# Kernel tuning notes

Hardware: AMD Instinct MI355X
Metric: run time of the kernel (lower is better)

## Reference

```python
import jax, jax.numpy as jnp
import numpy as np

N_HEADS = 16

def _rotate_half(t):
    d = t.shape[-1] // 2
    return jnp.concatenate([-t[..., d:], t[..., :d]], axis=-1)

def _apply_rope(t, cos, sin):
    # t: [B,S,H,dh], cos/sin: [S,1,dh] broadcast over B and H
    return t * cos + _rotate_half(t) * sin

def setup_inputs() -> dict:
    key = jax.random.key(0)
    ks = jax.random.split(key, 7)
    B, S, D = 2, 2048, 2048
    dh = D // N_HEADS
    scale = 1.0 / np.sqrt(D)
    return {
        "x": jax.random.normal(ks[0], (B, S, D), dtype=jnp.float32),
        "rope_cos": jax.random.uniform(ks[1], (S, dh), dtype=jnp.float32),
        "rope_sin": jax.random.uniform(ks[2], (S, dh), dtype=jnp.float32),
        "Wq": jax.random.normal(ks[3], (D, D), dtype=jnp.float32) * scale,
        "Wk": jax.random.normal(ks[4], (D, D), dtype=jnp.float32) * scale,
        "Wv": jax.random.normal(ks[5], (D, D), dtype=jnp.float32) * scale,
        "Wo": jax.random.normal(ks[6], (D, D), dtype=jnp.float32) * scale,
    }

def reference(x, rope_cos, rope_sin, Wq, Wk, Wv, Wo):
    B, S, D = x.shape
    H = N_HEADS
    dh = D // H
    # QKV projections (nn.Linear: x @ W.T), reshape to heads
    q = (x @ Wq.T).reshape(B, S, H, dh)
    k = (x @ Wk.T).reshape(B, S, H, dh)
    v = (x @ Wv.T).reshape(B, S, H, dh)
    cos = rope_cos[:, None, :]  # [S,1,dh]
    sin = rope_sin[:, None, :]
    q = _apply_rope(q, cos, sin)
    k = _apply_rope(k, cos, sin)
    # Attention: [B,H,S,S] scores, scaled softmax
    scores = jnp.einsum("bqhd,bkhd->bhqk", q, k) / jnp.sqrt(jnp.asarray(dh, dtype=x.dtype))
    probs = jax.nn.softmax(scores, axis=-1)
    out = jnp.einsum("bhqk,bkhd->bqhd", probs, v).reshape(B, S, D)
    return out @ Wo.T
```

## Files before the change

### kernel.cpp

```cpp
#include <hip/hip_runtime.h>
#include <hip/hip_bf16.h>

typedef unsigned short u16;
typedef __bf16 bf16x8 __attribute__((ext_vector_type(8)));
typedef float f32x4 __attribute__((ext_vector_type(4)));

__device__ __forceinline__ float bf2f(u16 u) {
  union { unsigned int i; float f; } v; v.i = ((unsigned int)u) << 16; return v.f;
}
__device__ __forceinline__ u16 f2bf(float f) {
  union { float f; unsigned int i; } v; v.f = f;
  unsigned int r = v.i + 0x7fffu + ((v.i >> 16) & 1u);
  return (u16)(r >> 16);
}
__device__ __forceinline__ unsigned cvtpk(float lo, float hi) {
  unsigned r;
  asm("v_cvt_pk_bf16_f32 %0, %1, %2" : "=v"(r) : "v"(lo), "v"(hi));
  return r;
}

__device__ __forceinline__ void async_load16(void* lds, const void* g) {
  __builtin_amdgcn_global_load_lds((const __attribute__((address_space(1))) void*)g,
                                   (__attribute__((address_space(3))) void*)lds, 16, 0, 0);
}

__global__ void convert_all(const float* __restrict__ x, const float* __restrict__ Wq,
                            const float* __restrict__ Wk, const float* __restrict__ Wv,
                            const float* __restrict__ Wo, u16* __restrict__ xb,
                            u16* __restrict__ Wqkb, u16* __restrict__ Wvb,
                            u16* __restrict__ Wob) {
  int bid = blockIdx.x;
  const float* src;
  u16* dst;
  int off;
  if (bid < 8192)       { src = x;  dst = xb;              off = bid; }
  else if (bid < 12288) { src = Wq; dst = Wqkb;            off = bid - 8192; }
  else if (bid < 16384) { src = Wk; dst = Wqkb + 4194304;  off = bid - 12288; }
  else if (bid < 20480) { src = Wv; dst = Wvb;             off = bid - 16384; }
  else                  { src = Wo; dst = Wob;             off = bid - 20480; }
  int i = off * 1024 + threadIdx.x * 4;
  float4 v = *(const float4*)(src + i);
  ushort4 o;
  o.x = f2bf(v.x); o.y = f2bf(v.y); o.z = f2bf(v.z); o.w = f2bf(v.w);
  *(ushort4*)(dst + i) = o;
}

template <int OUT_F32, int ROPE>
__device__ __forceinline__ void gemm_tile_body(const u16* __restrict__ A,
                                               const u16* __restrict__ Bm,
                                               void* __restrict__ C, int M, int N, int K,
                                               int swz, u16* sA, u16* sB,
                                               const float* __restrict__ cosb,
                                               const float* __restrict__ sinb,
                                               float qscale) {
  const int nTn = N >> 7;
  int tm = swz / nTn, tn = swz % nTn;
  const int t = threadIdx.x;
  const int w = t >> 6, l = t & 63;
  const int wr = w >> 1, wc = w & 1;
  const int lr = l & 15, lh = l >> 4;
  const size_t row0 = (size_t)tm * 128, col0 = (size_t)tn * 128;

  f32x4 zero = {0.f, 0.f, 0.f, 0.f};
  f32x4 acc[4][4];
#pragma unroll
  for (int i = 0; i < 4; ++i)
#pragma unroll
    for (int j = 0; j < 4; ++j) acc[i][j] = zero;

  const u16* Ag = A + row0 * K;
  const u16* Bg = Bm + col0 * K;

  for (int k0 = 0; k0 < K; k0 += 32) {
#pragma unroll
    for (int i = 0; i < 2; ++i) {
      int c = i * 256 + t;
      int r = c >> 2, kk = (c & 3) << 3;
      async_load16(sA + (((size_t)i * 256 + w * 64) << 3), Ag + (size_t)r * K + k0 + kk);
      async_load16(sB + (((size_t)i * 256 + w * 64) << 3), Bg + (size_t)r * K + k0 + kk);
    }
    __syncthreads();
    bf16x8 af[4], bfr[4];
#pragma unroll
    for (int mi = 0; mi < 4; ++mi)
      af[mi] = *reinterpret_cast<const bf16x8*>(sA + (wr * 64 + mi * 16 + lr) * 32 + lh * 8);
#pragma unroll
    for (int ni = 0; ni < 4; ++ni) {
      int colf = wc * 32 + (ni & 1) * 16 + (ni >> 1) * 64;
      bfr[ni] = *reinterpret_cast<const bf16x8*>(sB + (colf + lr) * 32 + lh * 8);
    }
#pragma unroll
    for (int mi = 0; mi < 4; ++mi)
#pragma unroll
      for (int ni = 0; ni < 4; ++ni)
        acc[mi][ni] = __builtin_amdgcn_mfma_f32_16x16x32_bf16(af[mi], bfr[ni], acc[mi][ni], 0, 0, 0);
    __syncthreads();
  }

  if (ROPE) {
    float scale = (tn < 16) ? qscale : 1.0f;
#pragma unroll
    for (int mi = 0; mi < 4; ++mi)
#pragma unroll
      for (int r = 0; r < 4; ++r) {
        size_t row = row0 + wr * 64 + mi * 16 + lh * 4 + r;
        int s = (int)(row & 2047);
        const float* cr = cosb + s * 128;
        const float* sr = sinb + s * 128;
#pragma unroll
        for (int ni = 0; ni < 2; ++ni) {
          int dlo = wc * 32 + ni * 16 + lr;
          float v0 = acc[mi][ni][r];
          float v1 = acc[mi][ni + 2][r];
          float o0 = (v0 * cr[dlo] - v1 * sr[dlo]) * scale;
          float o1 = (v1 * cr[64 + dlo] + v0 * sr[64 + dlo]) * scale;
          ((u16*)C)[row * N + col0 + dlo]      = f2bf(o0);
          ((u16*)C)[row * N + col0 + 64 + dlo] = f2bf(o1);
        }
      }
  } else {
#pragma unroll
    for (int mi = 0; mi < 4; ++mi)
#pragma unroll
      for (int ni = 0; ni < 4; ++ni)
#pragma unroll
        for (int r = 0; r < 4; ++r) {
          size_t row = row0 + wr * 64 + mi * 16 + lh * 4 + r;
          size_t col = col0 + wc * 32 + (ni & 1) * 16 + (ni >> 1) * 64 + lr;
          float v = acc[mi][ni][r];
          if (OUT_F32)
            ((float*)C)[row * N + col] = v;
          else
            ((u16*)C)[row * N + col] = f2bf(v);
        }
  }
}

__global__ __launch_bounds__(256)
void gemm_qkv(const u16* __restrict__ xb, const u16* __restrict__ Wqkb,
              const u16* __restrict__ Wvb, u16* __restrict__ QKb, u16* __restrict__ VTb,
              const float* __restrict__ cosb, const float* __restrict__ sinb, float qscale) {
  __shared__ __align__(16) u16 sA[128 * 32];
  __shared__ __align__(16) u16 sB[128 * 32];
  int bid = blockIdx.x;
  if (bid < 1024) {
    int swz = (bid & 7) * 128 + (bid >> 3);
    gemm_tile_body<0, 1>(xb, Wqkb, QKb, 4096, 4096, 2048, swz, sA, sB, cosb, sinb, qscale);
  } else {
    int b2 = bid - 1024;
    int swz = (b2 & 7) * 64 + (b2 >> 3);
    gemm_tile_body<0, 0>(Wvb, xb, VTb, 2048, 4096, 2048, swz, sA, sB, nullptr, nullptr, 0.f);
  }
}

__global__ __launch_bounds__(256)
void gemm_o(const u16* __restrict__ Ob, const u16* __restrict__ Wob, float* __restrict__ out) {
  __shared__ __align__(16) u16 sA[128 * 32];
  __shared__ __align__(16) u16 sB[128 * 32];
  int bid = blockIdx.x;
  int swz = (bid & 7) * 64 + (bid >> 3);
  gemm_tile_body<1, 0>(Ob, Wob, (void*)out, 4096, 2048, 2048, swz, sA, sB, nullptr, nullptr, 0.f);
}

__global__ __launch_bounds__(256, 2)
void attn_kernel(const u16* __restrict__ QKb, const u16* __restrict__ VT,
                 u16* __restrict__ Ob) {
  __shared__ __align__(16) u16 sK[2][64 * 128];
  __shared__ __align__(16) u16 sV[2][128 * 64];
  __shared__ __align__(16) u16 sP[4][32 * 64];

  int id = blockIdx.x;
  int swz = (id & 7) * 64 + (id >> 3);
  int bh = swz >> 4;
  int qb = swz & 15;
  int b = bh >> 4, h = bh & 15;
  int t = threadIdx.x, w = t >> 6, l = t & 63;
  int lr = l & 15, lh = l >> 4;
  int lr7 = lr & 7;
  int q0 = qb * 128;

  const u16* Kbase = QKb + (size_t)(b * 2048) * 4096 + 2048 + h * 128;
  const u16* Vbase = VT + (size_t)(h * 128) * 4096 + b * 2048;
  u16* sPw = sP[w];

  bf16x8 aq[2][4];
#pragma unroll
  for (int qf = 0; qf < 2; ++qf) {
    size_t qrow = (size_t)(b * 2048 + q0 + w * 32 + qf * 16 + lr) * 4096 + h * 128;
#pragma unroll
    for (int c = 0; c < 4; ++c)
      aq[qf][c] = *reinterpret_cast<const bf16x8*>(QKb + qrow + c * 32 + lh * 8);
  }

  f32x4 zero = {0.f, 0.f, 0.f, 0.f};
  f32x4 acc_o[2][8];
#pragma unroll
  for (int qf = 0; qf < 2; ++qf)
#pragma unroll
    for (int d = 0; d < 8; ++d) acc_o[qf][d] = zero;
  float m_row[2] = {-1e30f, -1e30f};
  float l_row[2] = {0.f, 0.f};

  auto stage = [&](int buf, int kt2) {
    const u16* Kt = Kbase + (size_t)(kt2 * 64) * 4096;
    const u16* Vt = Vbase + kt2 * 64;
#pragma unroll
    for (int it = 0; it < 4; ++it) {
      int o = it * 4096 + t * 16;
      int rowK = o >> 8;
      int cbK = (o & 255) ^ ((rowK & 7) << 4);
      async_load16((u16*)sK[buf] + (o >> 1), Kt + (size_t)rowK * 4096 + (cbK >> 1));
      int rowV = o >> 7;
      int cbV = (o & 127) ^ ((rowV & 7) << 4);
      async_load16((u16*)sV[buf] + (o >> 1), Vt + (size_t)rowV * 4096 + (cbV >> 1));
    }
  };

  stage(0, 0);
  __syncthreads();
  int cur = 0;

  for (int kt = 0; kt < 32; ++kt) {
    if (kt < 31) stage(cur ^ 1, kt + 1);

    const u16* sKc = sK[cur];
    const u16* sVc = sV[cur];

    f32x4 sacc[2][4];
#pragma unroll
    for (int qf = 0; qf < 2; ++qf)
#pragma unroll
      for (int g = 0; g < 4; ++g) sacc[qf][g] = zero;
#pragma unroll
    for (int g = 0; g < 4; ++g) {
      int row = g * 16 + lr;
      int xr = lr7 << 4;
#pragma unroll
      for (int c = 0; c < 4; ++c) {
        int cb = (c * 64 + lh * 16) ^ xr;
        bf16x8 bk = *reinterpret_cast<const bf16x8*>(sKc + row * 128 + (cb >> 1));
        sacc[0][g] = __builtin_amdgcn_mfma_f32_16x16x32_bf16(bk, aq[0][c], sacc[0][g], 0, 0, 0);
        sacc[1][g] = __builtin_amdgcn_mfma_f32_16x16x32_bf16(bk, aq[1][c], sacc[1][g], 0, 0, 0);
      }
    }

#pragma unroll
    for (int qf = 0; qf < 2; ++qf) {
      f32x4 m4;
#pragma unroll
      for (int e = 0; e < 4; ++e)
        m4[e] = fmaxf(fmaxf(sacc[qf][0][e], sacc[qf][1][e]),
                      fmaxf(sacc[qf][2][e], sacc[qf][3][e]));
      float mx = fmaxf(fmaxf(m4[0], m4[1]), fmaxf(m4[2], m4[3]));
      mx = fmaxf(mx, __shfl_xor(mx, 16));
      mx = fmaxf(mx, __shfl_xor(mx, 32));
      float mo = m_row[qf];
      if (!__all(mx <= mo + 8.f)) {
        float mn = fmaxf(mo, mx);
        float al = __builtin_amdgcn_exp2f(mo - mn);
        m_row[qf] = mn;
        l_row[qf] *= al;
#pragma unroll
        for (int d = 0; d < 8; ++d) acc_o[qf][d] *= al;
      }
      float mn = m_row[qf];
#pragma unroll
      for (int g = 0; g < 4; ++g)
#pragma unroll
        for (int e = 0; e < 4; ++e)
          sacc[qf][g][e] = __builtin_amdgcn_exp2f(sacc[qf][g][e] - mn);
      f32x4 s4;
#pragma unroll
      for (int e = 0; e < 4; ++e)
        s4[e] = (sacc[qf][0][e] + sacc[qf][1][e]) + (sacc[qf][2][e] + sacc[qf][3][e]);
      float rs = (s4[0] + s4[1]) + (s4[2] + s4[3]);
      rs += __shfl_xor(rs, 16);
      rs += __shfl_xor(rs, 32);
      l_row[qf] += rs;

      int rowb = (qf * 16 + lr) * 128;
      int xw = lr7 << 4;
#pragma unroll
      for (int g = 0; g < 4; ++g) {
        uint2 pw;
        pw.x = cvtpk(sacc[qf][g][0], sacc[qf][g][1]);
        pw.y = cvtpk(sacc[qf][g][2], sacc[qf][g][3]);
        int cb = (g * 32 + lh * 8) ^ xw;
        *reinterpret_cast<uint2*>(reinterpret_cast<char*>(sPw) + rowb + cb) = pw;
      }
    }

    bf16x8 bp[2][2];
#pragma unroll
    for (int qf = 0; qf < 2; ++qf) {
      int rowb = (qf * 16 + lr) * 128;
      int xr = lr7 << 4;
#pragma unroll
      for (int c2 = 0; c2 < 2; ++c2) {
        int cb = (c2 * 64 + lh * 16) ^ xr;
        bp[qf][c2] = *reinterpret_cast<const bf16x8*>(
            reinterpret_cast<const char*>(sPw) + rowb + cb);
      }
    }
#pragma unroll
    for (int c2 = 0; c2 < 2; ++c2) {
#pragma unroll
      for (int d = 0; d < 8; ++d) {
        int row = d * 16 + lr;
        int cb = (c2 * 64 + lh * 16) ^ (lr7 << 4);
        bf16x8 bv = *reinterpret_cast<const bf16x8*>(sVc + row * 64 + (cb >> 1));
        acc_o[0][d] = __builtin_amdgcn_mfma_f32_16x16x32_bf16(bv, bp[0][c2], acc_o[0][d], 0, 0, 0);
        acc_o[1][d] = __builtin_amdgcn_mfma_f32_16x16x32_bf16(bv, bp[1][c2], acc_o[1][d], 0, 0, 0);
      }
    }

    __syncthreads();
    cur ^= 1;
  }

#pragma unroll
  for (int qf = 0; qf < 2; ++qf) {
    float inv = 1.f / l_row[qf];
    size_t qrow = (size_t)(b * 2048 + q0 + w * 32 + qf * 16 + lr) * 2048 + h * 128;
#pragma unroll
    for (int d = 0; d < 8; ++d) {
      ushort4 o;
      o.x = f2bf(acc_o[qf][d][0] * inv);
      o.y = f2bf(acc_o[qf][d][1] * inv);
      o.z = f2bf(acc_o[qf][d][2] * inv);
      o.w = f2bf(acc_o[qf][d][3] * inv);
      *reinterpret_cast<ushort4*>(Ob + qrow + d * 16 + lh * 4) = o;
    }
  }
}

extern "C" void kernel_launch(void* const* d_in, const int* in_sizes, int n_in,
                              void* d_out, int out_size, void* d_ws, size_t ws_size,
                              hipStream_t stream) {
  const float* x  = (const float*)d_in[0];
  const float* rc = (const float*)d_in[1];
  const float* rs = (const float*)d_in[2];
  const float* Wq = (const float*)d_in[3];
  const float* Wk = (const float*)d_in[4];
  const float* Wv = (const float*)d_in[5];
  const float* Wo = (const float*)d_in[6];
  float* out = (float*)d_out;
  char* ws = (char*)d_ws;
  const size_t MB = 1024 * 1024;
  u16* xb   = (u16*)(ws);
  u16* Wqkb = (u16*)(ws + 16 * MB);
  u16* Wvb  = (u16*)(ws + 32 * MB);
  u16* Wob  = (u16*)(ws + 40 * MB);
  u16* QKb  = (u16*)(ws + 48 * MB);
  u16* VTb  = (u16*)(ws + 80 * MB);
  u16* Ob   = (u16*)(ws + 16 * MB);

  convert_all<<<24576, 256, 0, stream>>>(x, Wq, Wk, Wv, Wo, xb, Wqkb, Wvb, Wob);

  const float qscale = 0.08838834764831845f * 1.4426950408889634f;
  gemm_qkv<<<1536, 256, 0, stream>>>(xb, Wqkb, Wvb, QKb, VTb, rc, rs, qscale);

  attn_kernel<<<512, 256, 0, stream>>>(QKb, VTb, Ob);

  gemm_o<<<512, 256, 0, stream>>>(Ob, Wob, out);
}
```

Measured before the change: 283.5 us.

## Replace QKV GEMM with 256x256-tile, 4-stage async-pipelined 512-thread kernel

The fused QKV projection now uses 256x256 output tiles with 8 waves per block. A 4-deep ring of LDS stages is filled with async global-to-LDS loads and gated by vmcnt waits plus a single barrier per k-step, replacing the single-buffered two-barrier loop. MFMA sections are bracketed with raised wave priority. The aim is to hide global load latency and raise arithmetic intensity per LDS byte. The cost is 128KB of LDS, higher register pressure from 32 accumulators per lane, and only 384 blocks, which may underfill the GPU. The output-projection GEMM keeps the old body with a simplified column mapping.

```diff
diff --git a/kernel.cpp b/kernel.cpp
--- a/kernel.cpp
+++ b/kernel.cpp
@@ -45,14 +45,129 @@
   *(ushort4*)(dst + i) = o;
 }
 
-template <int OUT_F32, int ROPE>
+template <int ROPE>
+__device__ __forceinline__ void gemm256_body(const u16* __restrict__ A,
+                                             const u16* __restrict__ Bm,
+                                             u16* __restrict__ C, int M, int N, int K,
+                                             int tm, int tn, u16* lds,
+                                             const float* __restrict__ cosb,
+                                             const float* __restrict__ sinb,
+                                             float qscale) {
+  const int t = threadIdx.x;
+  const int w = t >> 6, l = t & 63;
+  const int wm = w >> 2, wn = w & 3;
+  const int lr = l & 15, lh = l >> 4;
+  const size_t row0 = (size_t)tm * 256, col0 = (size_t)tn * 256;
+  const u16* Ag = A + row0 * K;
+  const u16* Bg = Bm + col0 * K;
+
+  const int ra = t >> 2, kc = (t & 3) << 3;
+  auto stage = [&](int s) {
+    u16* dst = lds + (s & 3) * 16384;
+    const size_t koff = (size_t)s * 32 + kc;
+    async_load16(dst + t * 8,         Ag + (size_t)ra * K + koff);
+    async_load16(dst + 4096 + t * 8,  Ag + (size_t)(ra + 128) * K + koff);
+    async_load16(dst + 8192 + t * 8,  Bg + (size_t)ra * K + koff);
+    async_load16(dst + 12288 + t * 8, Bg + (size_t)(ra + 128) * K + koff);
+  };
+
+  f32x4 acc[8][4];
+#pragma unroll
+  for (int i = 0; i < 8; ++i)
+#pragma unroll
+    for (int j = 0; j < 4; ++j) acc[i][j] = (f32x4){0.f, 0.f, 0.f, 0.f};
+
+  const int NK = K >> 5;
+  stage(0); stage(1); stage(2);
+
+  for (int s = 0; s < NK; ++s) {
+    if (s + 2 < NK)      asm volatile("s_waitcnt vmcnt(8)" ::: "memory");
+    else if (s + 1 < NK) asm volatile("s_waitcnt vmcnt(4)" ::: "memory");
+    else                 asm volatile("s_waitcnt vmcnt(0)" ::: "memory");
+    __builtin_amdgcn_s_barrier();
+    asm volatile("" ::: "memory");
+    if (s + 3 < NK) stage(s + 3);
+
+    const u16* sub = lds + (s & 3) * 16384;
+    bf16x8 af[8], bfv[4];
+#pragma unroll
+    for (int mi = 0; mi < 8; ++mi)
+      af[mi] = *reinterpret_cast<const bf16x8*>(sub + (wm * 128 + mi * 16 + lr) * 32 + lh * 8);
+#pragma unroll
+    for (int ni = 0; ni < 4; ++ni) {
+      int colf = ROPE ? ((wn >> 1) * 128 + (wn & 1) * 32 + (ni >> 1) * 64 + (ni & 1) * 16)
+                      : (wn * 64 + ni * 16);
+      bfv[ni] = *reinterpret_cast<const bf16x8*>(sub + 8192 + (colf + lr) * 32 + lh * 8);
+    }
+    __builtin_amdgcn_s_setprio(1);
+#pragma unroll
+    for (int mi = 0; mi < 8; ++mi)
+#pragma unroll
+      for (int ni = 0; ni < 4; ++ni)
+        acc[mi][ni] = __builtin_amdgcn_mfma_f32_16x16x32_bf16(af[mi], bfv[ni], acc[mi][ni], 0, 0, 0);
+    __builtin_amdgcn_s_setprio(0);
+  }
+
+  if (ROPE) {
+    float scale = (2 * tn + (wn >> 1)) < 16 ? qscale : 1.0f;
+    size_t colbase = col0 + (wn >> 1) * 128;
+#pragma unroll
+    for (int mi = 0; mi < 8; ++mi)
+#pragma unroll
+      for (int r = 0; r < 4; ++r) {
+        size_t row = row0 + wm * 128 + mi * 16 + lh * 4 + r;
+        int si = (int)(row & 2047);
+        const float* cr = cosb + si * 128;
+        const float* sr = sinb + si * 128;
+#pragma unroll
+        for (int ni = 0; ni < 2; ++ni) {
+          int dlo = (wn & 1) * 32 + ni * 16 + lr;
+          float v0 = acc[mi][ni][r];
+          float v1 = acc[mi][ni + 2][r];
+          float o0 = (v0 * cr[dlo] - v1 * sr[dlo]) * scale;
+          float o1 = (v1 * cr[64 + dlo] + v0 * sr[64 + dlo]) * scale;
+          C[row * N + colbase + dlo]      = f2bf(o0);
+          C[row * N + colbase + 64 + dlo] = f2bf(o1);
+        }
+      }
+  } else {
+#pragma unroll
+    for (int mi = 0; mi < 8; ++mi)
+#pragma unroll
+      for (int ni = 0; ni < 4; ++ni)
+#pragma unroll
+        for (int r = 0; r < 4; ++r) {
+          size_t row = row0 + wm * 128 + mi * 16 + lh * 4 + r;
+          size_t col = col0 + wn * 64 + ni * 16 + lr;
+          C[row * N + col] = f2bf(acc[mi][ni][r]);
+        }
+  }
+}
+
+__global__ __launch_bounds__(512, 2)
+void gemm_qkv256(const u16* __restrict__ xb, const u16* __restrict__ Wqkb,
+                 const u16* __restrict__ Wvb, u16* __restrict__ QKb, u16* __restrict__ VTb,
+                 const float* __restrict__ cosb, const float* __restrict__ sinb,
+                 float qscale) {
+  __shared__ __align__(16) u16 lds[4 * 16384];
+  int bid = blockIdx.x;
+  if (bid < 256) {
+    int swz = (bid & 7) * 32 + (bid >> 3);
+    gemm256_body<1>(xb, Wqkb, QKb, 4096, 4096, 2048, swz >> 4, swz & 15, lds,
+                    cosb, sinb, qscale);
+  } else {
+    int b2 = bid - 256;
+    int swz = (b2 & 7) * 16 + (b2 >> 3);
+    gemm256_body<0>(Wvb, xb, VTb, 2048, 4096, 2048, swz >> 4, swz & 15, lds,
+                    nullptr, nullptr, 0.f);
+  }
+}
+
+template <int OUT_F32>
 __device__ __forceinline__ void gemm_tile_body(const u16* __restrict__ A,
                                                const u16* __restrict__ Bm,
                                                void* __restrict__ C, int M, int N, int K,
-                                               int swz, u16* sA, u16* sB,
-                                               const float* __restrict__ cosb,
-                                               const float* __restrict__ sinb,
-                                               float qscale) {
+                                               int swz, u16* sA, u16* sB) {
   const int nTn = N >> 7;
   int tm = swz / nTn, tn = swz % nTn;
   const int t = threadIdx.x;
@@ -85,10 +200,8 @@
     for (int mi = 0; mi < 4; ++mi)
       af[mi] = *reinterpret_cast<const bf16x8*>(sA + (wr * 64 + mi * 16 + lr) * 32 + lh * 8);
 #pragma unroll
-    for (int ni = 0; ni < 4; ++ni) {
-      int colf = wc * 32 + (ni & 1) * 16 + (ni >> 1) * 64;
-      bfr[ni] = *reinterpret_cast<const bf16x8*>(sB + (colf + lr) * 32 + lh * 8);
-    }
+    for (int ni = 0; ni < 4; ++ni)
+      bfr[ni] = *reinterpret_cast<const bf16x8*>(sB + (wc * 64 + ni * 16 + lr) * 32 + lh * 8);
 #pragma unroll
     for (int mi = 0; mi < 4; ++mi)
 #pragma unroll
@@ -97,60 +210,20 @@
     __syncthreads();
   }
 
-  if (ROPE) {
-    float scale = (tn < 16) ? qscale : 1.0f;
-#pragma unroll
-    for (int mi = 0; mi < 4; ++mi)
+#pragma unroll
+  for (int mi = 0; mi < 4; ++mi)
+#pragma unroll
+    for (int ni = 0; ni < 4; ++ni)
 #pragma unroll
       for (int r = 0; r < 4; ++r) {
         size_t row = row0 + wr * 64 + mi * 16 + lh * 4 + r;
-        int s = (int)(row & 2047);
-        const float* cr = cosb + s * 128;
-        const float* sr = sinb + s * 128;
-#pragma unroll
-        for (int ni = 0; ni < 2; ++ni) {
-          int dlo = wc * 32 + ni * 16 + lr;
-          float v0 = acc[mi][ni][r];
-          float v1 = acc[mi][ni + 2][r];
-          float o0 = (v0 * cr[dlo] - v1 * sr[dlo]) * scale;
-          float o1 = (v1 * cr[64 + dlo] + v0 * sr[64 + dlo]) * scale;
-          ((u16*)C)[row * N + col0 + dlo]      = f2bf(o0);
-          ((u16*)C)[row * N + col0 + 64 + dlo] = f2bf(o1);
-        }
-      }
-  } else {
-#pragma unroll
-    for (int mi = 0; mi < 4; ++mi)
-#pragma unroll
-      for (int ni = 0; ni < 4; ++ni)
-#pragma unroll
-        for (int r = 0; r < 4; ++r) {
-          size_t row = row0 + wr * 64 + mi * 16 + lh * 4 + r;
-          size_t col = col0 + wc * 32 + (ni & 1) * 16 + (ni >> 1) * 64 + lr;
-          float v = acc[mi][ni][r];
-          if (OUT_F32)
-            ((float*)C)[row * N + col] = v;
-          else
-            ((u16*)C)[row * N + col] = f2bf(v);
-        }
-  }
-}
-
-__global__ __launch_bounds__(256)
-void gemm_qkv(const u16* __restrict__ xb, const u16* __restrict__ Wqkb,
-              const u16* __restrict__ Wvb, u16* __restrict__ QKb, u16* __restrict__ VTb,
-              const float* __restrict__ cosb, const float* __restrict__ sinb, float qscale) {
-  __shared__ __align__(16) u16 sA[128 * 32];
-  __shared__ __align__(16) u16 sB[128 * 32];
-  int bid = blockIdx.x;
-  if (bid < 1024) {
-    int swz = (bid & 7) * 128 + (bid >> 3);
-    gemm_tile_body<0, 1>(xb, Wqkb, QKb, 4096, 4096, 2048, swz, sA, sB, cosb, sinb, qscale);
-  } else {
-    int b2 = bid - 1024;
-    int swz = (b2 & 7) * 64 + (b2 >> 3);
-    gemm_tile_body<0, 0>(Wvb, xb, VTb, 2048, 4096, 2048, swz, sA, sB, nullptr, nullptr, 0.f);
-  }
+        size_t col = col0 + wc * 64 + ni * 16 + lr;
+        float v = acc[mi][ni][r];
+        if (OUT_F32)
+          ((float*)C)[row * N + col] = v;
+        else
+          ((u16*)C)[row * N + col] = f2bf(v);
+      }
 }
 
 __global__ __launch_bounds__(256)
@@ -159,7 +232,7 @@
   __shared__ __align__(16) u16 sB[128 * 32];
   int bid = blockIdx.x;
   int swz = (bid & 7) * 64 + (bid >> 3);
-  gemm_tile_body<1, 0>(Ob, Wob, (void*)out, 4096, 2048, 2048, swz, sA, sB, nullptr, nullptr, 0.f);
+  gemm_tile_body<1>(Ob, Wob, (void*)out, 4096, 2048, 2048, swz, sA, sB);
 }
 
 __global__ __launch_bounds__(256, 2)
@@ -358,7 +431,7 @@
   convert_all<<<24576, 256, 0, stream>>>(x, Wq, Wk, Wv, Wo, xb, Wqkb, Wvb, Wob);
 
   const float qscale = 0.08838834764831845f * 1.4426950408889634f;
-  gemm_qkv<<<1536, 256, 0, stream>>>(xb, Wqkb, Wvb, QKb, VTb, rc, rs, qscale);
+  gemm_qkv256<<<384, 512, 0, stream>>>(xb, Wqkb, Wvb, QKb, VTb, rc, rs, qscale);
 
   attn_kernel<<<512, 256, 0, stream>>>(QKb, VTb, Ob);
 
```

After: 281.8 us. About the same (-0.6%).
